# Kernel tuning notes

Hardware: AMD Instinct MI355X
Metric: run time of the kernel (lower is better)

## Reference

```python
import math
import jax, jax.numpy as jnp
import numpy as np

B, N, E, H, DH = 2, 1024, 512, 8, 64
KMAX, WIN = 8, 32
LOG_N = 11              # ceil(log2(max_seq_len+1)) for max_seq_len=1024
DP = LOG_N + 1          # depth-indexed parameter banks 0..log_n
LEVELS = 10             # log2(N): merge levels 1..10 (full binary tree over N leaves)
LN_EPS = 1e-5


def _build_static():
    """Static segment-tree layout: per-position causal cover sets + flat node slots."""
    leaf_start = 1 << LOG_N
    offs = [0]
    for d in range(LEVELS):
        offs.append(offs[-1] + (N >> d))
    M = offs[LEVELS] + 1  # levels 0..LEVELS, total 2N-1 nodes
    kvalid = np.ones(M, np.int32)
    for d in range(LEVELS + 1):
        kvalid[offs[d]:offs[d] + (N >> d)] = min(1 << d, KMAX)
    covers = []
    for pos in range(N):  # prefix [0..pos-1]
        l, r = leaf_start, leaf_start + pos
        out = []
        while l < r:
            if l & 1:
                out.append(l); l += 1
            if r & 1:
                r -= 1; out.append(r)
            l >>= 1; r >>= 1
        covers.append(out)
    S = max(1, max(len(c) for c in covers))
    ci = np.zeros((N, S), np.int32)
    cd = np.zeros((N, S), np.int32)
    cm = np.zeros((N, S), bool)
    for i, c in enumerate(covers):
        for s, node in enumerate(c):
            d = LOG_N - int(math.floor(math.log2(node)))
            ci[i, s] = offs[d] + (node - (leaf_start >> d))
            cd[i, s] = d
            cm[i, s] = True
    return ci, cd, cm, kvalid


def setup_inputs() -> dict:
    key = jax.random.key(0)
    ks = jax.random.split(key, 16)
    nrm = lambda k, s, sc=0.02: jax.random.normal(k, s, jnp.float32) * sc
    ci, cd, cm, kv = _build_static()
    return {
        "x": jax.random.normal(ks[0], (B, N, E), jnp.float32),
        "qW": nrm(ks[1], (E, E)), "qb": jnp.zeros((E,), jnp.float32),
        "vW": nrm(ks[2], (E, E)), "vb": jnp.zeros((E,), jnp.float32),
        "oW": nrm(ks[3], (E, E)), "ob": jnp.zeros((E,), jnp.float32),
        "klW": nrm(ks[4], (E, E)), "klb": jnp.zeros((E,), jnp.float32),
        "vlW": nrm(ks[5], (E, E)), "vlb": jnp.zeros((E,), jnp.float32),
        "gW": nrm(ks[6], (E, E)), "gb": jnp.full((E,), 2.0, jnp.float32),
        "ddqW": nrm(ks[7], (DP, DH, DH)),
        "ddqT": jnp.linspace(0.5, 4.0, DP).astype(jnp.float32),
        "wfreq": jnp.linspace(0.3, 4.0, H).astype(jnp.float32),
        "wdamp": jnp.linspace(-3.0, 0.5, H).astype(jnp.float32),
        "wphase": jnp.linspace(0.0, math.pi, H).astype(jnp.float32),
        "glW": nrm(ks[8], (DP, DH, 2 * DH)), "glb": jnp.full((DP, DH), 0.5, jnp.float32),
        "grW": nrm(ks[9], (DP, DH, 2 * DH)), "grb": jnp.full((DP, DH), 0.5, jnp.float32),
        "pq": nrm(ks[10], (DP, KMAX, DH)),
        "lnG": jnp.ones((DP, DH), jnp.float32), "lnB": jnp.zeros((DP, DH), jnp.float32),
        "skA": jnp.full((DP,), 0.1, jnp.float32),
        "skW": nrm(ks[11], (DP, DH, DH)),
        "coup": jnp.eye(H, dtype=jnp.float32)[None] + nrm(ks[12], (DP, H, H), 0.01),
        "cov_idx": jnp.asarray(ci), "cov_depth": jnp.asarray(cd),
        "cov_mask": jnp.asarray(cm), "kvalid": jnp.asarray(kv),
    }


def reference(x, qW, qb, vW, vb, oW, ob, klW, klb, vlW, vlb, gW, gb, ddqW, ddqT,
              wfreq, wdamp, wphase, glW, glb, grW, grb, pq, lnG, lnB, skA, skW,
              coup, cov_idx, cov_depth, cov_mask, kvalid):
    q = (x @ qW.T + qb).reshape(B, N, H, DH)
    v = (x @ vW.T + vb).reshape(B, N, H, DH)

    # ---- local exact causal window attention ----
    k_loc = (x @ klW.T + klb).reshape(B, N, H, DH)
    v_loc = (x @ vlW.T + vlb).reshape(B, N, H, DH)
    j = jnp.arange(N)[:, None] - jnp.arange(WIN)[None, :]  # (N, W) key positions
    valid = j >= 0
    jc = jnp.clip(j, 0, N - 1)
    kg = k_loc[:, jc]  # (B,N,W,H,DH)
    vg = v_loc[:, jc]
    sc = jnp.einsum('bnhd,bnwhd->bhnw', q, kg) / math.sqrt(DH)
    sc = jnp.where(valid[None, None], sc, -1e9)
    local = jnp.einsum('bhnw,bnwhd->bnhd', jax.nn.softmax(sc, axis=-1), vg)

    # ---- build segment tree, vectorized per depth level ----
    alpha_b = jax.nn.softplus(wdamp)
    cur = jnp.transpose(v, (0, 2, 1, 3))[:, :, :, None, :]  # leaves (B,H,N,1,DH)
    levels = [cur]
    for d in range(1, LEVELS + 1):
        fL, fR = cur[:, :, 0::2], cur[:, :, 1::2]  # (B,H,n,K,DH)
        # depth-scaled complex rotation (alpha_d*dt = alpha, omega_d*dt = omega)
        scale = float(1 << (LOG_N - d))
        dec = jnp.exp(-(alpha_b / scale) * scale)
        ang = (wfreq / scale) * scale + (wphase + d * (math.pi / 4.0))
        pr = (dec * jnp.cos(ang)).reshape(1, H, 1, 1, 1)
        pi_ = (dec * jnp.sin(ang)).reshape(1, H, 1, 1, 1)
        d2 = DH // 2
        fre, fim = fR[..., :d2], fR[..., d2:]
        rot = jnp.concatenate([pr * fre - pi_ * fim, pi_ * fre + pr * fim], -1)
        lm, rm = fL.mean(3), rot.mean(3)  # (B,H,n,DH)
        gin = jnp.concatenate([lm, rm], -1)
        gl = jax.nn.sigmoid(gin @ glW[d].T + glb[d])[..., None, :]
        gr = jax.nn.sigmoid(gin @ grW[d].T + grb[d])[..., None, :]
        bank = jnp.concatenate([fL * gl, rot * gr], 3)  # (B,H,n,2K,DH)
        kp = min(2 * cur.shape[3], KMAX)
        att = jax.nn.softmax(
            jnp.einsum('qd,bhnkd->bhnqk', pq[d, :kp], bank) / math.sqrt(DH), -1)
        par = jnp.einsum('bhnqk,bhnkd->bhnqd', att, bank)
        mu = par.mean(-1, keepdims=True)
        par = (par - mu) * jax.lax.rsqrt(par.var(-1, keepdims=True) + LN_EPS)
        par = par * lnG[d] + lnB[d]
        par = par + jax.nn.sigmoid(skA[d]) * (lm @ skW[d].T)[..., None, :]
        cur = jnp.einsum('ij,bjnkd->binkd', jax.nn.softmax(coup[d], -1), par)
        levels.append(cur)

    # flat node bank padded to KMAX vectors per node: (B,H,M,KMAX,DH)
    bank_all = jnp.concatenate(
        [jnp.pad(lv, ((0, 0), (0, 0), (0, 0), (0, KMAX - lv.shape[3]), (0, 0)))
         for lv in levels], axis=2)

    # ---- depth-decomposed query over causal cover sets ----
    Qall = q[None] + jnp.einsum('bnhd,ped->pbnhe', q, ddqW)  # (DP,B,N,H,DH)
    sc_d = 1.0 / ((jax.nn.softplus(ddqT) + 1e-6) * math.sqrt(DH))
    Qt = jnp.transpose(Qall, (2, 0, 1, 3, 4))  # (N,DP,B,H,DH)
    Qg = Qt[jnp.arange(N)[:, None], cov_depth]  # (N,S,B,H,DH)
    bg = bank_all[:, :, cov_idx]  # (B,H,N,S,KMAX,DH)
    scores = jnp.einsum('nsbhd,bhnskd->bhnsk', Qg, bg)
    scores = scores * sc_d[cov_depth][None, None, :, :, None]
    kmsk = jnp.arange(KMAX)[None, None] < kvalid[cov_idx][:, :, None]
    msk = cov_mask[:, :, None] & kmsk  # (N,S,KMAX)
    scores = jnp.where(msk[None, None], scores, -1e9)
    aw = jax.nn.softmax(scores.reshape(B, H, N, -1), -1).reshape(scores.shape)
    tree_out = jnp.einsum('bhnsk,bhnskd->bnhd', aw, bg)
    tree_out = jnp.where(cov_mask.any(1)[None, :, None, None], tree_out, 0.0)

    gate = jax.nn.sigmoid(x @ gW.T + gb).reshape(B, N, H, DH)
    out = (local + gate * tree_out).reshape(B, N, E)
    return out @ oW.T + ob
```

## Files before the change

kernel.cpp:

```cpp
#include <hip/hip_runtime.h>
#include <math.h>

#define B_ 2
#define N_ 1024
#define H_ 8
#define TOTV 5104

typedef __attribute__((ext_vector_type(8))) short bf16x8;
typedef __attribute__((ext_vector_type(4))) float f32x4;

__device__ __constant__ int VBASE[11] = {0,1024,2048,3072,4096,4608,4864,4992,5056,5088,5104};

constexpr int vbase_of(int d) {
  int v = 0;
  for (int i = 0; i < d; ++i) v += (1024 >> i) * ((i >= 3) ? 8 : (1 << i));
  return v;
}

__device__ __forceinline__ float wsum(float v) {
  v += __shfl_xor(v, 1);  v += __shfl_xor(v, 2);  v += __shfl_xor(v, 4);
  v += __shfl_xor(v, 8);  v += __shfl_xor(v, 16); v += __shfl_xor(v, 32);
  return v;
}
__device__ __forceinline__ float sigmoidf_(float x) { return 1.f / (1.f + __expf(-x)); }
__device__ __forceinline__ unsigned short f2b(float f) {
  unsigned u = __float_as_uint(f);
  return (unsigned short)((u + 0x7FFFu + ((u >> 16) & 1u)) >> 16);
}
__device__ __forceinline__ float b2f(unsigned short h) {
  return __uint_as_float(((unsigned)h) << 16);
}
__device__ __forceinline__ float dot4(float4 a, float4 b) {
  return a.x*b.x + a.y*b.y + a.z*b.z + a.w*b.w;
}
__device__ __forceinline__ float rl(float v, int l) {
  return __uint_as_float(__builtin_amdgcn_readlane(__float_as_uint(v), l));
}
__device__ __forceinline__ void gl16(const unsigned short* g, unsigned short* l) {
  __builtin_amdgcn_global_load_lds(
      (const __attribute__((address_space(1))) unsigned int*)g,
      (__attribute__((address_space(3))) unsigned int*)l, 16, 0, 0);
}

__global__ void prep_kernel(const float* __restrict__ x,
                            const float* __restrict__ w0, const float* __restrict__ w1,
                            const float* __restrict__ w2, const float* __restrict__ w3,
                            const float* __restrict__ w4, const float* __restrict__ oW,
                            const float* __restrict__ ddqW, const float* __restrict__ ddqT,
                            unsigned short* __restrict__ A2x, unsigned short* __restrict__ B2w,
                            unsigned short* __restrict__ B2o, unsigned short* __restrict__ B2q)
{
  const int bx = blockIdx.x;
  const int tid = threadIdx.x;
  if (bx < 1024) {
    int i = (bx * 256 + tid) * 4;
    int m = i >> 9, k = i & 511;
    float4 f = *(const float4*)(x + i);
    float fv[4] = {f.x, f.y, f.z, f.w};
    unsigned short h[4], l[4];
#pragma unroll
    for (int j = 0; j < 4; ++j) { h[j] = f2b(fv[j]); l[j] = f2b(fv[j] - b2f(h[j])); }
    size_t base = (size_t)m * 1536;
    ushort4 hv = {h[0], h[1], h[2], h[3]};
    ushort4 lv = {l[0], l[1], l[2], l[3]};
    *(ushort4*)(A2x + base + k) = hv;
    *(ushort4*)(A2x + base + 512 + k) = lv;
    *(ushort4*)(A2x + base + 1024 + k) = hv;
  } else if (bx < 2304) {
    int i = ((bx - 1024) * 256 + tid) * 4;
    int nrow = i >> 9, k = i & 511;
    int sel = nrow >> 9;
    const float* w = sel == 0 ? w0 : sel == 1 ? w1 : sel == 2 ? w2 : sel == 3 ? w3 : w4;
    float4 f = *(const float4*)(w + (size_t)(nrow & 511) * 512 + k);
    float fv[4] = {f.x, f.y, f.z, f.w};
    unsigned short h[4], l[4];
#pragma unroll
    for (int j = 0; j < 4; ++j) { h[j] = f2b(fv[j]); l[j] = f2b(fv[j] - b2f(h[j])); }
    size_t base = (size_t)nrow * 1536;
    ushort4 hv = {h[0], h[1], h[2], h[3]};
    ushort4 lv = {l[0], l[1], l[2], l[3]};
    *(ushort4*)(B2w + base + k) = hv;
    *(ushort4*)(B2w + base + 512 + k) = hv;
    *(ushort4*)(B2w + base + 1024 + k) = lv;
  } else if (bx < 2560) {
    int i = ((bx - 2304) * 256 + tid) * 4;
    int m = i >> 9, k = i & 511;
    float4 f = *(const float4*)(oW + i);
    float fv[4] = {f.x, f.y, f.z, f.w};
    unsigned short h[4], l[4];
#pragma unroll
    for (int j = 0; j < 4; ++j) { h[j] = f2b(fv[j]); l[j] = f2b(fv[j] - b2f(h[j])); }
    size_t base = (size_t)m * 1536;
    ushort4 hv = {h[0], h[1], h[2], h[3]};
    ushort4 lv = {l[0], l[1], l[2], l[3]};
    *(ushort4*)(B2o + base + k) = hv;
    *(ushort4*)(B2o + base + 512 + k) = hv;
    *(ushort4*)(B2o + base + 1024 + k) = lv;
  } else {
    int i = (bx - 2560) * 256 + tid;
    int row = i >> 6, e = i & 63;
    int p = row >> 6, o = row & 63;
    float t = ddqT[p];
    float sp = log1pf(__expf(t));
    float scd = 1.f / ((sp + 1e-6f) * 8.0f);
    float w = (ddqW[(size_t)(p * 64 + o) * 64 + e] + (o == e ? 1.f : 0.f)) * scd;
    unsigned short h = f2b(w);
    unsigned short l = f2b(w - b2f(h));
    size_t base = (size_t)row * 192;
    B2q[base + e] = h; B2q[base + 64 + e] = h; B2q[base + 128 + e] = l;
  }
}

template<int MODE, int BM>
__global__ __launch_bounds__(256)
void gemm_mfma(const unsigned short* __restrict__ A2, const unsigned short* __restrict__ B2,
               const int K3,
               const float* __restrict__ bq, const float* __restrict__ bv,
               const float* __restrict__ bkl, const float* __restrict__ bvl,
               const float* __restrict__ bgt,
               float* __restrict__ qbuf, float* __restrict__ bank,
               float* __restrict__ klbuf, float* __restrict__ vlbuf,
               float* __restrict__ gatebuf, float* __restrict__ Qs,
               float* __restrict__ oout, const float* __restrict__ ob,
               unsigned short* __restrict__ A2q)
{
  constexpr int MREP = BM / 32;
  __shared__ __align__(16) unsigned short Alds[BM * 32];
  __shared__ __align__(16) unsigned short Blds[64 * 32];
  const int tid = threadIdx.x;
  const int wave = tid >> 6, lane = tid & 63;
  const int wr = wave >> 1, wc = wave & 1;
  const int row0 = blockIdx.y * BM, col0 = blockIdx.x * 64;

  f32x4 acc[MREP][2];
#pragma unroll
  for (int i = 0; i < MREP; ++i)
#pragma unroll
    for (int j = 0; j < 2; ++j) acc[i][j] = (f32x4){0.f, 0.f, 0.f, 0.f};

  const int rIn = lane >> 2;
  const int jIn = lane & 3;
  const int arow0 = (BM == 128 ? (2 * wave) * 16 : wave * 16) + rIn;
  const int arow1 = (2 * wave + 1) * 16 + rIn;
  const int brow  = wave * 16 + rIn;
  const unsigned short* aSrc0 = A2 + (size_t)(row0 + arow0) * K3 + ((jIn ^ ((arow0 >> 1) & 3)) << 3);
  const unsigned short* aSrc1 = A2 + (size_t)(row0 + (BM == 128 ? arow1 : arow0)) * K3
                                   + ((jIn ^ (((BM == 128 ? arow1 : arow0) >> 1) & 3)) << 3);
  const unsigned short* bSrc  = B2 + (size_t)(col0 + brow) * K3 + ((jIn ^ ((brow >> 1) & 3)) << 3);
  unsigned short* aDst0 = Alds + (BM == 128 ? (2 * wave) * 512 : wave * 512);
  unsigned short* aDst1 = Alds + (BM == 128 ? (2 * wave + 1) * 512 : wave * 512);
  unsigned short* bDst  = Blds + wave * 512;

  const int lrow = lane & 15, kslot = lane >> 4;

  for (int kt = 0; kt < K3; kt += 32) {
    __syncthreads();
    gl16(aSrc0 + kt, aDst0);
    if constexpr (BM == 128) gl16(aSrc1 + kt, aDst1);
    gl16(bSrc + kt, bDst);
    __syncthreads();

    bf16x8 af[MREP], bf[2];
#pragma unroll
    for (int m = 0; m < MREP; ++m) {
      const int r = wr * (BM / 2) + m * 16 + lrow;
      af[m] = *(const bf16x8*)(Alds + r * 32 + ((kslot ^ ((r >> 1) & 3)) << 3));
    }
#pragma unroll
    for (int n = 0; n < 2; ++n) {
      const int r = wc * 32 + n * 16 + lrow;
      bf[n] = *(const bf16x8*)(Blds + r * 32 + ((kslot ^ ((r >> 1) & 3)) << 3));
    }
#pragma unroll
    for (int m = 0; m < MREP; ++m)
#pragma unroll
      for (int n = 0; n < 2; ++n)
        acc[m][n] = __builtin_amdgcn_mfma_f32_16x16x32_bf16(af[m], bf[n], acc[m][n], 0, 0, 0);
  }

#pragma unroll
  for (int m = 0; m < MREP; ++m)
#pragma unroll
    for (int n = 0; n < 2; ++n)
#pragma unroll
      for (int r = 0; r < 4; ++r) {
        const int row = row0 + wr * (BM / 2) + m * 16 + (lane >> 4) * 4 + r;
        const int col = col0 + wc * 32 + n * 16 + (lane & 15);
        float v = acc[m][n][r];
        if (MODE == 0) {
          const int sel = col >> 9;
          const int c = col & 511;
          const int bb = row >> 10, nn = row & 1023;
          if (sel == 0) {
            float vv = v + bq[c];
            qbuf[(size_t)row * 512 + c] = vv;
            unsigned short hi = f2b(vv), lo = f2b(vv - b2f(hi));
            size_t mq = (size_t)row * 8 + (c >> 6);
            int kq = c & 63;
            A2q[mq * 192 + kq] = hi;
            A2q[mq * 192 + 64 + kq] = lo;
            A2q[mq * 192 + 128 + kq] = hi;
          } else if (sel == 1) {
            bank[((size_t)(bb * 8 + (c >> 6)) * TOTV + nn) * 64 + (c & 63)] = v + bv[c];
          } else if (sel == 2) {
            klbuf[(size_t)row * 512 + c] = v + bkl[c];
          } else if (sel == 3) {
            vlbuf[(size_t)row * 512 + c] = v + bvl[c];
          } else {
            gatebuf[(size_t)row * 512 + c] = sigmoidf_(v + bgt[c]);
          }
        } else if (MODE == 1) {
          Qs[((size_t)(col >> 6) * 16384 + row) * 64 + (col & 63)] = v;
        } else {
          oout[(size_t)row * 512 + col] = v + ob[col];
        }
      }
}

template<int D, int NPB>
__global__ __launch_bounds__(512)
void level5(const float* __restrict__ glW, const float* __restrict__ glb,
            const float* __restrict__ grW, const float* __restrict__ grb,
            const float* __restrict__ pq, const float* __restrict__ lnG,
            const float* __restrict__ lnB, const float* __restrict__ skA,
            const float* __restrict__ skW, const float* __restrict__ coup,
            const float* __restrict__ wfreq, const float* __restrict__ wdamp,
            const float* __restrict__ wphase, float* __restrict__ bank)
{
  constexpr int KPREV = ((D - 1) >= 3) ? 8 : (1 << (D - 1));
  constexpr int SLOTS = 2 * KPREV;
  constexpr int KP = (D >= 3) ? 8 : (1 << D);
  constexpr bool TP = (D >= 3);
  constexpr int VB_PREV = vbase_of(D - 1);
  constexpr int VB_CUR  = vbase_of(D);

  __shared__ __align__(8)  float wpk[128 * 130];
  __shared__ float sklds[64 * 65];
  __shared__ float parlds[8][KP][64];
  __shared__ __align__(16) float slds[TP ? 8 * SLOTS * 68 : 1];
  __shared__ float wlds[TP ? 8 * KP * 17 : 1];
  __shared__ __align__(16) float pqlds[TP ? KP * 68 : 1];

  const int tid = threadIdx.x;
  const int h = tid >> 6, lane = tid & 63;
  const int b = blockIdx.y;

  for (int i = tid; i < 64 * 128; i += 512) {
    int o = i >> 7, e = i & 127;
    wpk[e * 130 + 2 * o]     = glW[(size_t)D * 8192 + i];
    wpk[e * 130 + 2 * o + 1] = grW[(size_t)D * 8192 + i];
  }
  for (int i = tid; i < 64 * 64; i += 512) {
    int o = i >> 6, e = i & 63;
    sklds[e * 65 + o] = skW[(size_t)D * 4096 + i];
  }
  if constexpr (TP) {
    for (int i = tid; i < KP * 64; i += 512)
      pqlds[(i >> 6) * 68 + (i & 63)] = pq[(size_t)D * 512 + i];
  }
  __syncthreads();

  const float alpha = log1pf(__expf(wdamp[h]));
  const float dec = __expf(-alpha);
  const float ang = wfreq[h] + wphase[h] + (float)D * 0.78539816339744831f;
  const float pr  = dec * cosf(ang);
  const float pim = dec * sinf(ang);
  const float glbv = glb[D * 64 + lane], grbv = grb[D * 64 + lane];
  const float lnGv = lnG[D * 64 + lane], lnBv = lnB[D * 64 + lane];
  const float sig_sk = sigmoidf_(skA[D]);
  float cw[8];
  float cmx = -1e30f;
#pragma unroll
  for (int j = 0; j < 8; ++j) { cw[j] = coup[(size_t)(D * 8 + h) * 8 + j]; cmx = fmaxf(cmx, cw[j]); }
  float cs = 0.f;
#pragma unroll
  for (int j = 0; j < 8; ++j) { cw[j] = __expf(cw[j] - cmx); cs += cw[j]; }
  const float cinv = 1.f / cs;

  const size_t bh = (size_t)(b * H_ + h);
  const float* prevb = bank + (bh * TOTV + VB_PREV) * 64;
  float* curb = bank + (bh * TOTV + VB_CUR) * 64;

  for (int nn = 0; nn < NPB; ++nn) {
    const int node = blockIdx.x * NPB + nn;
    float par[KP];
    float fL[KPREV], rot[KPREV];
    {
      float lm = 0.f, rm = 0.f;
#pragma unroll
      for (int k = 0; k < KPREV; ++k) {
        fL[k] = prevb[(size_t)((2 * node) * KPREV + k) * 64 + lane];
        float fr = prevb[(size_t)((2 * node + 1) * KPREV + k) * 64 + lane];
        float partner = __shfl_xor(fr, 32);
        rot[k] = (lane < 32) ? (pr * fr - pim * partner) : (pim * partner + pr * fr);
        lm += fL[k]; rm += rot[k];
      }
      lm *= (1.f / KPREV); rm *= (1.f / KPREV);

      float gl = glbv, gr = grbv, sk = 0.f;
#pragma unroll
      for (int e = 0; e < 64; ++e) {
        float g = rl(lm, e);
        float2 w2 = *(const float2*)&wpk[e * 130 + 2 * lane];
        gl += g * w2.x;
        gr += g * w2.y;
        sk += g * sklds[e * 65 + lane];
      }
#pragma unroll
      for (int e = 0; e < 64; ++e) {
        float g = rl(rm, e);
        float2 w2 = *(const float2*)&wpk[(64 + e) * 130 + 2 * lane];
        gl += g * w2.x;
        gr += g * w2.y;
      }
      gl = sigmoidf_(gl); gr = sigmoidf_(gr);

      float slot[SLOTS];
#pragma unroll
      for (int k = 0; k < KPREV; ++k) { slot[k] = fL[k] * gl; slot[KPREV + k] = rot[k] * gr; }

      if constexpr (!TP) {
        float pqv[KP];
#pragma unroll
        for (int qi = 0; qi < KP; ++qi) pqv[qi] = pq[(size_t)(D * 8 + qi) * 64 + lane];
#pragma unroll
        for (int qi = 0; qi < KP; ++qi) {
          float lg[SLOTS];
          float mx = -1e30f;
#pragma unroll
          for (int kk = 0; kk < SLOTS; ++kk) {
            lg[kk] = wsum(pqv[qi] * slot[kk]) * 0.125f;
            mx = fmaxf(mx, lg[kk]);
          }
          float den = 0.f, pv = 0.f;
#pragma unroll
          for (int kk = 0; kk < SLOTS; ++kk) {
            float w = __expf(lg[kk] - mx);
            den += w; pv += w * slot[kk];
          }
          par[qi] = pv / den;
        }
      } else {
        float* sl = &slds[h * SLOTS * 68];
#pragma unroll
        for (int kk = 0; kk < SLOTS; ++kk) sl[kk * 68 + lane] = slot[kk];
        constexpr int PAIRS = KP * SLOTS;
        const int kk0 = lane & (SLOTS - 1);
        const int qg  = lane / SLOTS;
        float s0 = 0.f, s1 = 0.f;
        {
          const float4* sv = (const float4*)&sl[kk0 * 68];
          const float4* q0 = (const float4*)&pqlds[qg * 68];
#pragma unroll
          for (int e = 0; e < 16; ++e) s0 += dot4(q0[e], sv[e]);
          if constexpr (PAIRS == 128) {
            const float4* q1 = (const float4*)&pqlds[(qg + 4) * 68];
#pragma unroll
            for (int e = 0; e < 16; ++e) s1 += dot4(q1[e], sv[e]);
          }
        }
        s0 *= 0.125f; s1 *= 0.125f;
        float m0 = s0, m1 = s1;
#pragma unroll
        for (int o = 1; o < SLOTS; o <<= 1) {
          m0 = fmaxf(m0, __shfl_xor(m0, o));
          if constexpr (PAIRS == 128) m1 = fmaxf(m1, __shfl_xor(m1, o));
        }
        float e0 = __expf(s0 - m0), e1 = (PAIRS == 128) ? __expf(s1 - m1) : 0.f;
        float d0 = e0, d1 = e1;
#pragma unroll
        for (int o = 1; o < SLOTS; o <<= 1) {
          d0 += __shfl_xor(d0, o);
          if constexpr (PAIRS == 128) d1 += __shfl_xor(d1, o);
        }
        float* wld = &wlds[h * KP * 17];
        wld[qg * 17 + kk0] = e0 / d0;
        if constexpr (PAIRS == 128) wld[(qg + 4) * 17 + kk0] = e1 / d1;
#pragma unroll
        for (int qi = 0; qi < KP; ++qi) {
          float acc2 = 0.f;
#pragma unroll
          for (int kk = 0; kk < SLOTS; ++kk) acc2 += wld[qi * 17 + kk] * slot[kk];
          par[qi] = acc2;
        }
      }

#pragma unroll
      for (int qi = 0; qi < KP; ++qi) {
        float mu = wsum(par[qi]) * (1.f / 64.f);
        float dv = par[qi] - mu;
        float var = wsum(dv * dv) * (1.f / 64.f);
        float nv = dv * rsqrtf(var + 1e-5f);
        par[qi] = nv * lnGv + lnBv + sig_sk * sk;
        parlds[h][qi][lane] = par[qi];
      }
    }
    __syncthreads();
#pragma unroll
    for (int qi = 0; qi < KP; ++qi) {
      float o = 0.f;
#pragma unroll
      for (int j = 0; j < 8; ++j) o += cw[j] * parlds[j][qi][lane];
      curb[(size_t)(node * KP + qi) * 64 + lane] = o * cinv;
    }
    __syncthreads();
  }
}

__global__ __launch_bounds__(512)
void combine3(const float* __restrict__ qbuf, const float* __restrict__ klbuf,
              const float* __restrict__ vlbuf, const float* __restrict__ gatebuf,
              const float* __restrict__ bank, const float* __restrict__ Qs,
              unsigned short* __restrict__ A2o)
{
  const int flat = blockIdx.y * 1024 + blockIdx.x;
  const int swz = (flat & 7) * 256 + (flat >> 3);
  const int n = swz & 1023;
  const int b = swz >> 10;
  const int h = threadIdx.x >> 6;
  const int lane = threadIdx.x & 63;
  __shared__ int pair_ro[64];
  __shared__ int pair_sl[64];
  __shared__ int sdepth[16];
  __shared__ int PS[2];
  __shared__ __align__(16) float Qlds[8][10][68];
  __shared__ __align__(16) float qlds[8][64];
  __shared__ float sclds[8][64];

  if (threadIdx.x == 0) {
    int l = 2048, r = 2048 + n;
    int cnt = 0, sc = 0;
    while (l < r) {
      if (l & 1) {
        int m = l++;
        int j = 31 - __clz(m);
        int d = 11 - j;
        int local = m - (1 << j);
        int kv = (d >= 3) ? 8 : (1 << d);
        sdepth[sc] = d;
        int vb = VBASE[d] + local * kv;
        for (int k = 0; k < kv; ++k) { pair_ro[cnt] = (vb + k) * 64; pair_sl[cnt] = sc; ++cnt; }
        ++sc;
      }
      if (r & 1) {
        int m = --r;
        int j = 31 - __clz(m);
        int d = 11 - j;
        int local = m - (1 << j);
        int kv = (d >= 3) ? 8 : (1 << d);
        sdepth[sc] = d;
        int vb = VBASE[d] + local * kv;
        for (int k = 0; k < kv; ++k) { pair_ro[cnt] = (vb + k) * 64; pair_sl[cnt] = sc; ++cnt; }
        ++sc;
      }
      l >>= 1; r >>= 1;
    }
    PS[0] = cnt; PS[1] = sc;
    for (int k = cnt; k < 64; ++k) { pair_ro[k] = 0; pair_sl[k] = 0; }
  }
  const size_t vbase = ((size_t)(b * N_ + n) * H_ + h) * 64;
  qlds[h][lane] = qbuf[vbase + lane];
  __syncthreads();
  const int P = PS[0], S = PS[1];

  for (int s = 0; s < S; ++s)
    Qlds[h][s][lane] = Qs[((size_t)sdepth[s] * 16384 + (size_t)(b * N_ + n) * H_ + h) * 64 + lane];

  const int w = lane & 31, half = lane >> 5;
  const int wmax = (n + 1 < 32) ? (n + 1) : 32;
  float scl = 0.f;
  if (w < wmax) {
    const float4* k4 = (const float4*)(klbuf + vbase - (size_t)w * 512 + half * 32);
    const float4* q4 = (const float4*)&qlds[h][half * 32];
#pragma unroll
    for (int e = 0; e < 8; ++e) scl += dot4(q4[e], k4[e]);
  }
  scl += __shfl_xor(scl, 32);
  scl *= 0.125f;
  float sm = (w < wmax) ? scl : -1e30f;
  float mx = sm;
#pragma unroll
  for (int o = 1; o < 32; o <<= 1) mx = fmaxf(mx, __shfl_xor(mx, o));
  float le = (w < wmax) ? __expf(sm - mx) : 0.f;
  float den = le;
#pragma unroll
  for (int o = 1; o < 32; o <<= 1) den += __shfl_xor(den, o);
  float lp = le / den;
  float local = 0.f;
  if (n >= 31) {
#pragma unroll 8
    for (int ww = 0; ww < 32; ++ww) {
      float pw = __shfl(lp, ww);
      local += pw * vlbuf[vbase - (size_t)ww * 512 + lane];
    }
  } else {
    for (int ww = 0; ww < wmax; ++ww) {
      float pw = __shfl(lp, ww);
      local += pw * vlbuf[vbase - (size_t)ww * 512 + lane];
    }
  }

  const size_t bhbase = (size_t)(b * H_ + h) * TOTV * 64;
  float tree = 0.f;
  if (P > 0) {
    const int passes = (P + 15) >> 4;
    for (int t = 0; t < passes; ++t) {
      const int p = (t << 4) + (lane >> 2);
      const int c = lane & 3;
      float s = 0.f;
      if (p < P) {
        const float4* b4 = (const float4*)(bank + bhbase + pair_ro[p] + c * 16);
        const float4* q4 = (const float4*)&Qlds[h][pair_sl[p]][c * 16];
#pragma unroll
        for (int i = 0; i < 4; ++i) s += dot4(q4[i], b4[i]);
      }
      s += __shfl_xor(s, 1);
      s += __shfl_xor(s, 2);
      if (c == 0 && p < P) sclds[h][p] = s;
    }
    float logit = (lane < P) ? sclds[h][lane] : -1e30f;
    float tm = logit;
#pragma unroll
    for (int o = 1; o < 64; o <<= 1) tm = fmaxf(tm, __shfl_xor(tm, o));
    float te = (lane < P) ? __expf(logit - tm) : 0.f;
    float tden = te;
#pragma unroll
    for (int o = 1; o < 64; o <<= 1) tden += __shfl_xor(tden, o);
    float tw = te / tden;
    const int P4 = (P + 3) & ~3;
    for (int l2 = 0; l2 < P4; l2 += 4) {
      float w0_ = __shfl(tw, l2),     w1_ = __shfl(tw, l2 + 1);
      float w2_ = __shfl(tw, l2 + 2), w3_ = __shfl(tw, l2 + 3);
      float v0 = bank[bhbase + pair_ro[l2]     + lane];
      float v1 = bank[bhbase + pair_ro[l2 + 1] + lane];
      float v2 = bank[bhbase + pair_ro[l2 + 2] + lane];
      float v3 = bank[bhbase + pair_ro[l2 + 3] + lane];
      tree += w0_ * v0 + w1_ * v1 + w2_ * v2 + w3_ * v3;
    }
  }

  float g = gatebuf[vbase + lane];
  float v = local + g * tree;
  unsigned short hi = f2b(v), lo = f2b(v - b2f(hi));
  const size_t m = (size_t)(b * N_ + n);
  const int k = h * 64 + lane;
  A2o[m * 1536 + k] = hi;
  A2o[m * 1536 + 512 + k] = lo;
  A2o[m * 1536 + 1024 + k] = hi;
}

extern "C" void kernel_launch(void* const* d_in, const int* in_sizes, int n_in,
                              void* d_out, int out_size, void* d_ws, size_t ws_size,
                              hipStream_t stream)
{
  (void)in_sizes; (void)n_in; (void)out_size; (void)ws_size;
  const float* x     = (const float*)d_in[0];
  const float* qW    = (const float*)d_in[1];
  const float* qb    = (const float*)d_in[2];
  const float* vW    = (const float*)d_in[3];
  const float* vb    = (const float*)d_in[4];
  const float* oW    = (const float*)d_in[5];
  const float* ob    = (const float*)d_in[6];
  const float* klW   = (const float*)d_in[7];
  const float* klb   = (const float*)d_in[8];
  const float* vlW   = (const float*)d_in[9];
  const float* vlb   = (const float*)d_in[10];
  const float* gW    = (const float*)d_in[11];
  const float* gb    = (const float*)d_in[12];
  const float* ddqW  = (const float*)d_in[13];
  const float* ddqT  = (const float*)d_in[14];
  const float* wfreq = (const float*)d_in[15];
  const float* wdamp = (const float*)d_in[16];
  const float* wphase= (const float*)d_in[17];
  const float* glW   = (const float*)d_in[18];
  const float* glb   = (const float*)d_in[19];
  const float* grW   = (const float*)d_in[20];
  const float* grb   = (const float*)d_in[21];
  const float* pq    = (const float*)d_in[22];
  const float* lnG   = (const float*)d_in[23];
  const float* lnB   = (const float*)d_in[24];
  const float* skA   = (const float*)d_in[25];
  const float* skW   = (const float*)d_in[26];
  const float* coup  = (const float*)d_in[27];

  float* ws = (float*)d_ws;
  float* qbuf    = ws; ws += (size_t)2048 * 512;
  float* klbuf   = ws; ws += (size_t)2048 * 512;
  float* vlbuf   = ws; ws += (size_t)2048 * 512;
  float* gatebuf = ws; ws += (size_t)2048 * 512;
  float* bank    = ws; ws += (size_t)16 * TOTV * 64;
  float* Qs      = ws; ws += (size_t)10 * 16384 * 64;
  unsigned short* A2x = (unsigned short*)ws; ws += (size_t)2048 * 1536 / 2;
  unsigned short* B2w = (unsigned short*)ws; ws += (size_t)2560 * 1536 / 2;
  unsigned short* A2q = (unsigned short*)ws; ws += (size_t)16384 * 192 / 2;
  unsigned short* B2q = (unsigned short*)ws; ws += (size_t)640 * 192 / 2;
  unsigned short* A2o = (unsigned short*)ws; ws += (size_t)2048 * 1536 / 2;
  unsigned short* B2o = (unsigned short*)ws; ws += (size_t)512 * 1536 / 2;

  prep_kernel<<<2720, 256, 0, stream>>>(x, qW, vW, klW, vlW, gW, oW, ddqW, ddqT,
                                        A2x, B2w, B2o, B2q);

  gemm_mfma<0, 128><<<dim3(40, 16), 256, 0, stream>>>(A2x, B2w, 1536,
      qb, vb, klb, vlb, gb, qbuf, bank, klbuf, vlbuf, gatebuf,
      nullptr, nullptr, nullptr, A2q);

  gemm_mfma<1, 128><<<dim3(10, 128), 256, 0, stream>>>(A2q, B2q, 192,
      nullptr, nullptr, nullptr, nullptr, nullptr,
      nullptr, nullptr, nullptr, nullptr, nullptr, Qs, nullptr, nullptr, nullptr);

#define LVL(DD, NPB) level5<DD, NPB><<<dim3((1024 >> DD) / NPB, 2), 512, 0, stream>>>( \
      glW, glb, grW, grb, pq, lnG, lnB, skA, skW, coup, wfreq, wdamp, wphase, bank)
  LVL(1, 4); LVL(2, 2); LVL(3, 1); LVL(4, 1); LVL(5, 1);
  LVL(6, 1); LVL(7, 1); LVL(8, 1); LVL(9, 1);
#undef LVL

  combine3<<<dim3(1024, 2), 512, 0, stream>>>(qbuf, klbuf, vlbuf, gatebuf, bank, Qs, A2o);

  gemm_mfma<2, 64><<<dim3(8, 32), 256, 0, stream>>>(A2o, B2o, 1536,
      nullptr, nullptr, nullptr, nullptr, nullptr,
      nullptr, nullptr, nullptr, nullptr, nullptr, nullptr,
      (float*)d_out, ob, nullptr);
}
```

Before: 388.2 us.

## Fuse tree merge levels into one persistent kernel with grid barriers

Replaces nine separate per-level launches with a single persistent kernel of 128 blocks that loops over (batch, node) work items and separates levels with an atomic-counter grid barrier. Per-level weights are loaded into LDS before the barrier, so that load overlaps with other blocks finishing the previous level. The combine kernel also prefetches the 32 local-window value rows into registers and widens the tree-weighted gather to 8 loads per iteration. The goal is to remove launch overhead and the idle tails of the small late levels. In exchange, early levels run with fewer blocks than before, and the barrier depends on all 128 blocks being co-resident.

After: 498.6 us. 1.28x slower.

```diff
diff --git a/kernel.cpp b/kernel.cpp
--- a/kernel.cpp
+++ b/kernel.cpp
@@ -5,6 +5,7 @@
 #define N_ 1024
 #define H_ 8
 #define TOTV 5104
+#define LBLK 128
 
 typedef __attribute__((ext_vector_type(8))) short bf16x8;
 typedef __attribute__((ext_vector_type(4))) float f32x4;
@@ -40,6 +41,15 @@
   __builtin_amdgcn_global_load_lds(
       (const __attribute__((address_space(1))) unsigned int*)g,
       (__attribute__((address_space(3))) unsigned int*)l, 16, 0, 0);
+}
+__device__ __forceinline__ void grid_bar(int* bar, int slot) {
+  __syncthreads();
+  if (threadIdx.x == 0) {
+    __hip_atomic_fetch_add(&bar[slot], 1, __ATOMIC_ACQ_REL, __HIP_MEMORY_SCOPE_AGENT);
+    while (__hip_atomic_load(&bar[slot], __ATOMIC_ACQUIRE, __HIP_MEMORY_SCOPE_AGENT) < (int)gridDim.x)
+      __builtin_amdgcn_s_sleep(1);
+  }
+  __syncthreads();
 }
 
 __global__ void prep_kernel(const float* __restrict__ x,
@@ -217,15 +227,17 @@
       }
 }
 
-template<int D, int NPB>
-__global__ __launch_bounds__(512)
-void level5(const float* __restrict__ glW, const float* __restrict__ glb,
-            const float* __restrict__ grW, const float* __restrict__ grb,
-            const float* __restrict__ pq, const float* __restrict__ lnG,
-            const float* __restrict__ lnB, const float* __restrict__ skA,
-            const float* __restrict__ skW, const float* __restrict__ coup,
-            const float* __restrict__ wfreq, const float* __restrict__ wdamp,
-            const float* __restrict__ wphase, float* __restrict__ bank)
+template<int D>
+__device__ __forceinline__ void run_level(
+    const float* __restrict__ glW, const float* __restrict__ glb,
+    const float* __restrict__ grW, const float* __restrict__ grb,
+    const float* __restrict__ pq, const float* __restrict__ lnG,
+    const float* __restrict__ lnB, const float* __restrict__ skA,
+    const float* __restrict__ skW, const float* __restrict__ coup,
+    const float* __restrict__ wfreq, const float* __restrict__ wdamp,
+    const float* __restrict__ wphase, float* __restrict__ bank,
+    float* wpk, float* sklds, float* parlds, float* slds, float* wlds,
+    float* pqlds, int* bar)
 {
   constexpr int KPREV = ((D - 1) >= 3) ? 8 : (1 << (D - 1));
   constexpr int SLOTS = 2 * KPREV;
@@ -233,18 +245,12 @@
   constexpr bool TP = (D >= 3);
   constexpr int VB_PREV = vbase_of(D - 1);
   constexpr int VB_CUR  = vbase_of(D);
-
-  __shared__ __align__(8)  float wpk[128 * 130];
-  __shared__ float sklds[64 * 65];
-  __shared__ float parlds[8][KP][64];
-  __shared__ __align__(16) float slds[TP ? 8 * SLOTS * 68 : 1];
-  __shared__ float wlds[TP ? 8 * KP * 17 : 1];
-  __shared__ __align__(16) float pqlds[TP ? KP * 68 : 1];
+  constexpr int NODES = 1024 >> D;
 
   const int tid = threadIdx.x;
   const int h = tid >> 6, lane = tid & 63;
-  const int b = blockIdx.y;
-
+
+  __syncthreads();
   for (int i = tid; i < 64 * 128; i += 512) {
     int o = i >> 7, e = i & 127;
     wpk[e * 130 + 2 * o]     = glW[(size_t)D * 8192 + i];
@@ -258,6 +264,9 @@
     for (int i = tid; i < KP * 64; i += 512)
       pqlds[(i >> 6) * 68 + (i & 63)] = pq[(size_t)D * 512 + i];
   }
+  if constexpr (D > 1) grid_bar(bar, D - 2);
+  else __syncthreads();
+  if constexpr (D > 1) { } else { }
   __syncthreads();
 
   const float alpha = log1pf(__expf(wdamp[h]));
@@ -277,12 +286,13 @@
   for (int j = 0; j < 8; ++j) { cw[j] = __expf(cw[j] - cmx); cs += cw[j]; }
   const float cinv = 1.f / cs;
 
-  const size_t bh = (size_t)(b * H_ + h);
-  const float* prevb = bank + (bh * TOTV + VB_PREV) * 64;
-  float* curb = bank + (bh * TOTV + VB_CUR) * 64;
-
-  for (int nn = 0; nn < NPB; ++nn) {
-    const int node = blockIdx.x * NPB + nn;
+  for (int t = blockIdx.x; t < 2 * NODES; t += (int)gridDim.x) {
+    const int b = t & 1;
+    const int node = t >> 1;
+    const size_t bh = (size_t)(b * H_ + h);
+    const float* prevb = bank + (bh * TOTV + VB_PREV) * 64;
+    float* curb = bank + (bh * TOTV + VB_CUR) * 64;
+
     float par[KP];
     float fL[KPREV], rot[KPREV];
     {
@@ -341,7 +351,7 @@
           par[qi] = pv / den;
         }
       } else {
-        float* sl = &slds[h * SLOTS * 68];
+        float* sl = slds + h * (16 * 68);
 #pragma unroll
         for (int kk = 0; kk < SLOTS; ++kk) sl[kk * 68 + lane] = slot[kk];
         constexpr int PAIRS = KP * SLOTS;
@@ -373,7 +383,7 @@
           d0 += __shfl_xor(d0, o);
           if constexpr (PAIRS == 128) d1 += __shfl_xor(d1, o);
         }
-        float* wld = &wlds[h * KP * 17];
+        float* wld = wlds + h * (8 * 17);
         wld[qg * 17 + kk0] = e0 / d0;
         if constexpr (PAIRS == 128) wld[(qg + 4) * 17 + kk0] = e1 / d1;
 #pragma unroll
@@ -392,7 +402,7 @@
         float var = wsum(dv * dv) * (1.f / 64.f);
         float nv = dv * rsqrtf(var + 1e-5f);
         par[qi] = nv * lnGv + lnBv + sig_sk * sk;
-        parlds[h][qi][lane] = par[qi];
+        parlds[(h * 8 + qi) * 64 + lane] = par[qi];
       }
     }
     __syncthreads();
@@ -400,15 +410,38 @@
     for (int qi = 0; qi < KP; ++qi) {
       float o = 0.f;
 #pragma unroll
-      for (int j = 0; j < 8; ++j) o += cw[j] * parlds[j][qi][lane];
+      for (int j = 0; j < 8; ++j) o += cw[j] * parlds[(j * 8 + qi) * 64 + lane];
       curb[(size_t)(node * KP + qi) * 64 + lane] = o * cinv;
     }
     __syncthreads();
   }
 }
 
+__global__ __launch_bounds__(512, 1)
+void levels_fused(const float* __restrict__ glW, const float* __restrict__ glb,
+                  const float* __restrict__ grW, const float* __restrict__ grb,
+                  const float* __restrict__ pq, const float* __restrict__ lnG,
+                  const float* __restrict__ lnB, const float* __restrict__ skA,
+                  const float* __restrict__ skW, const float* __restrict__ coup,
+                  const float* __restrict__ wfreq, const float* __restrict__ wdamp,
+                  const float* __restrict__ wphase, float* __restrict__ bank,
+                  int* __restrict__ bar)
+{
+  __shared__ __align__(8)  float wpk[128 * 130];
+  __shared__ float sklds[64 * 65];
+  __shared__ float parlds[8 * 8 * 64];
+  __shared__ __align__(16) float slds[8 * 16 * 68];
+  __shared__ float wlds[8 * 8 * 17];
+  __shared__ __align__(16) float pqlds[8 * 68];
+
+#define RUNL(DD) run_level<DD>(glW, glb, grW, grb, pq, lnG, lnB, skA, skW, coup, \
+                               wfreq, wdamp, wphase, bank, wpk, sklds, parlds, slds, wlds, pqlds, bar)
+  RUNL(1); RUNL(2); RUNL(3); RUNL(4); RUNL(5); RUNL(6); RUNL(7); RUNL(8); RUNL(9);
+#undef RUNL
+}
+
 __global__ __launch_bounds__(512)
-void combine3(const float* __restrict__ qbuf, const float* __restrict__ klbuf,
+void combine4(const float* __restrict__ qbuf, const float* __restrict__ klbuf,
               const float* __restrict__ vlbuf, const float* __restrict__ gatebuf,
               const float* __restrict__ bank, const float* __restrict__ Qs,
               unsigned short* __restrict__ A2o)
@@ -468,6 +501,7 @@
 
   const int w = lane & 31, half = lane >> 5;
   const int wmax = (n + 1 < 32) ? (n + 1) : 32;
+  const bool full = (n >= 31);
   float scl = 0.f;
   if (w < wmax) {
     const float4* k4 = (const float4*)(klbuf + vbase - (size_t)w * 512 + half * 32);
@@ -475,6 +509,11 @@
 #pragma unroll
     for (int e = 0; e < 8; ++e) scl += dot4(q4[e], k4[e]);
   }
+  float vreg[32];
+  if (full) {
+#pragma unroll
+    for (int ww = 0; ww < 32; ++ww) vreg[ww] = vlbuf[vbase - (size_t)ww * 512 + lane];
+  }
   scl += __shfl_xor(scl, 32);
   scl *= 0.125f;
   float sm = (w < wmax) ? scl : -1e30f;
@@ -487,12 +526,9 @@
   for (int o = 1; o < 32; o <<= 1) den += __shfl_xor(den, o);
   float lp = le / den;
   float local = 0.f;
-  if (n >= 31) {
-#pragma unroll 8
-    for (int ww = 0; ww < 32; ++ww) {
-      float pw = __shfl(lp, ww);
-      local += pw * vlbuf[vbase - (size_t)ww * 512 + lane];
-    }
+  if (full) {
+#pragma unroll
+    for (int ww = 0; ww < 32; ++ww) local += __shfl(lp, ww) * vreg[ww];
   } else {
     for (int ww = 0; ww < wmax; ++ww) {
       float pw = __shfl(lp, ww);
@@ -527,15 +563,15 @@
 #pragma unroll
     for (int o = 1; o < 64; o <<= 1) tden += __shfl_xor(tden, o);
     float tw = te / tden;
-    const int P4 = (P + 3) & ~3;
-    for (int l2 = 0; l2 < P4; l2 += 4) {
-      float w0_ = __shfl(tw, l2),     w1_ = __shfl(tw, l2 + 1);
-      float w2_ = __shfl(tw, l2 + 2), w3_ = __shfl(tw, l2 + 3);
-      float v0 = bank[bhbase + pair_ro[l2]     + lane];
-      float v1 = bank[bhbase + pair_ro[l2 + 1] + lane];
-      float v2 = bank[bhbase + pair_ro[l2 + 2] + lane];
-      float v3 = bank[bhbase + pair_ro[l2 + 3] + lane];
-      tree += w0_ * v0 + w1_ * v1 + w2_ * v2 + w3_ * v3;
+    const int P8 = (P + 7) & ~7;
+    for (int l2 = 0; l2 < P8; l2 += 8) {
+      float v[8], wgt[8];
+#pragma unroll
+      for (int u = 0; u < 8; ++u) v[u] = bank[bhbase + pair_ro[l2 + u] + lane];
+#pragma unroll
+      for (int u = 0; u < 8; ++u) wgt[u] = __shfl(tw, l2 + u);
+#pragma unroll
+      for (int u = 0; u < 8; ++u) tree += wgt[u] * v[u];
     }
   }
 
@@ -596,6 +632,9 @@
   unsigned short* B2q = (unsigned short*)ws; ws += (size_t)640 * 192 / 2;
   unsigned short* A2o = (unsigned short*)ws; ws += (size_t)2048 * 1536 / 2;
   unsigned short* B2o = (unsigned short*)ws; ws += (size_t)512 * 1536 / 2;
+  int* bar = (int*)ws; ws += 16;
+
+  hipMemsetAsync(bar, 0, 16 * sizeof(int), stream);
 
   prep_kernel<<<2720, 256, 0, stream>>>(x, qW, vW, klW, vlW, gW, oW, ddqW, ddqT,
                                         A2x, B2w, B2o, B2q);
@@ -608,13 +647,10 @@
       nullptr, nullptr, nullptr, nullptr, nullptr,
       nullptr, nullptr, nullptr, nullptr, nullptr, Qs, nullptr, nullptr, nullptr);
 
-#define LVL(DD, NPB) level5<DD, NPB><<<dim3((1024 >> DD) / NPB, 2), 512, 0, stream>>>( \
-      glW, glb, grW, grb, pq, lnG, lnB, skA, skW, coup, wfreq, wdamp, wphase, bank)
-  LVL(1, 4); LVL(2, 2); LVL(3, 1); LVL(4, 1); LVL(5, 1);
-  LVL(6, 1); LVL(7, 1); LVL(8, 1); LVL(9, 1);
-#undef LVL
-
-  combine3<<<dim3(1024, 2), 512, 0, stream>>>(qbuf, klbuf, vlbuf, gatebuf, bank, Qs, A2o);
+  levels_fused<<<dim3(LBLK), 512, 0, stream>>>(glW, glb, grW, grb, pq, lnG, lnB,
+      skA, skW, coup, wfreq, wdamp, wphase, bank, bar);
+
+  combine4<<<dim3(1024, 2), 512, 0, stream>>>(qbuf, klbuf, vlbuf, gatebuf, bank, Qs, A2o);
 
   gemm_mfma<2, 64><<<dim3(8, 32), 256, 0, stream>>>(A2o, B2o, 1536,
       nullptr, nullptr, nullptr, nullptr, nullptr,
```
